# Performance work log

Measured on AMD Instinct MI355X. Metric: run time of the kernel, lower is better.

## Reference

```python
import jax, jax.numpy as jnp
import numpy as np

B, T, C, H = 2, 2048, 1024, 16
HD = C // H  # head_dim = 64


def setup_inputs() -> dict:
    key = jax.random.key(0)
    k1, k2, k3 = jax.random.split(key, 3)
    x = jax.random.normal(k1, (B, T, C), dtype=jnp.float32)
    w_attn = jax.random.normal(k2, (3 * C, C), dtype=jnp.float32) * 0.02
    w_proj = jax.random.normal(k3, (C, C), dtype=jnp.float32) * 0.02
    # RoPE frequencies: theta_i = 10000^(-2i/head_dim)
    inv_freq = 1.0 / (10000.0 ** (jnp.arange(0, HD, 2, dtype=jnp.float32) / HD))  # (HD//2,)
    angles = jnp.arange(T, dtype=jnp.float32)[:, None] * inv_freq[None, :]        # (T, HD//2)
    return {
        "x": x,
        "w_attn": w_attn,
        "w_proj": w_proj,
        "freqs_cos": jnp.cos(angles),
        "freqs_sin": jnp.sin(angles),
    }


def _rope(t, cos, sin):
    # t: (B, T, H, HD); cos/sin: (T, HD//2) broadcast to (1, T, 1, HD//2)
    te = t[..., 0::2]
    to = t[..., 1::2]
    c = cos[None, :, None, :]
    s = sin[None, :, None, :]
    re = te * c - to * s
    ro = te * s + to * c
    # interleave back: (..., HD//2, 2) -> (..., HD)
    return jnp.stack([re, ro], axis=-1).reshape(t.shape)


def reference(x, w_attn, w_proj, freqs_cos, freqs_sin):
    b, t, c = x.shape
    qkv = jnp.einsum('btc,fc->btf', x, w_attn)          # (B, T, 3C)
    q, k, v = jnp.split(qkv, 3, axis=2)
    q = q.reshape(b, t, H, HD)
    k = k.reshape(b, t, H, HD)
    v = v.reshape(b, t, H, HD)
    q = _rope(q, freqs_cos, freqs_sin)
    k = _rope(k, freqs_cos, freqs_sin)
    # causal SDPA
    scale = 1.0 / np.sqrt(HD).astype(np.float32)
    scores = jnp.einsum('bqhd,bkhd->bhqk', q, k) * scale  # (B, H, T, T)
    mask = jnp.tril(jnp.ones((t, t), dtype=bool))
    scores = jnp.where(mask[None, None, :, :], scores, jnp.finfo(scores.dtype).min)
    attn = jax.nn.softmax(scores, axis=-1)
    y = jnp.einsum('bhqk,bkhd->bqhd', attn, v).reshape(b, t, c)
    return jnp.einsum('btc,oc->bto', y, w_proj)
```

## Files before the change

kernel.cpp:

```cpp
#include <hip/hip_runtime.h>
#include <math.h>

#define B_  2
#define T_  2048
#define C_  1024
#define H_  16
#define HD_ 64
#define F3_ 3072

#define X4_   ((B_ * T_ * C_) / 4)
#define WA4_  ((F3_ * C_) / 4)
#define WP4_  ((C_ * C_) / 4)
#define TOT4_ (X4_ + WA4_ + WP4_)

typedef __attribute__((ext_vector_type(8))) __bf16 bf16x8;
typedef __attribute__((ext_vector_type(4))) float  f32x4;

__device__ __forceinline__ ushort f2bf(float f) {
  uint32_t u = __builtin_bit_cast(uint32_t, f);
  u += 0x7fff + ((u >> 16) & 1);
  return (ushort)(u >> 16);
}
__device__ __forceinline__ float bf2f(ushort u) {
  return __builtin_bit_cast(float, (uint32_t)u << 16);
}
__device__ __forceinline__ void gll16(void* lds, const void* g) {
  __builtin_amdgcn_global_load_lds(
      (const __attribute__((address_space(1))) void*)g,
      (__attribute__((address_space(3))) void*)lds, 16, 0, 0);
}

__global__ __launch_bounds__(256) void cvt_all(const float* __restrict__ x,
                                               const float* __restrict__ wa,
                                               const float* __restrict__ wp,
                                               ushort* __restrict__ out) {
  static_assert(X4_ == 1048576 && WA4_ == 786432 && WP4_ == 262144, "sizes");
  static_assert((X4_ % 256) == 0 && ((X4_ + WA4_) % 256) == 0, "block-uniform");
  int i = blockIdx.x * 256 + threadIdx.x;
  const float* src; int off;
  if (i < X4_)              { src = x;  off = i; }
  else if (i < X4_ + WA4_)  { src = wa; off = i - X4_; }
  else                      { src = wp; off = i - (X4_ + WA4_); }
  float4 v = ((const float4*)src)[off];
  ushort4 o;
  o.x = f2bf(v.x); o.y = f2bf(v.y); o.z = f2bf(v.z); o.w = f2bf(v.w);
  ((ushort4*)out)[i] = o;
}

template<int MODE>
__global__ __launch_bounds__(256) void gemm_mfma(
    const ushort* __restrict__ A, const ushort* __restrict__ Bm,
    void* __restrict__ Cout, ushort* __restrict__ vT,
    int M, int N, int K)
{
  __shared__ ushort As[128][64];
  __shared__ ushort Bs[128][64];
  const int tid  = threadIdx.x;
  const int lane = tid & 63, w = tid >> 6;
  const int wr = w >> 1, wc = w & 1;
  const int ll = lane & 15, lg = lane >> 4;
  const int r8 = lane >> 3;
  const int gc = ((lane & 7) ^ r8) << 3;
  const int m0 = blockIdx.x * 128, n0 = blockIdx.y * 128;

  f32x4 acc[4][4] = {};

  for (int k0 = 0; k0 < K; k0 += 64) {
    __syncthreads();
#pragma unroll
    for (int iss = 0; iss < 4; ++iss) {
      int rb = w * 32 + iss * 8;
      gll16(&As[rb][0], A  + (size_t)(m0 + rb + r8) * K + k0 + gc);
      gll16(&Bs[rb][0], Bm + (size_t)(n0 + rb + r8) * K + k0 + gc);
    }
    __syncthreads();
#pragma unroll
    for (int ks = 0; ks < 2; ++ks) {
      const int sw = ((ks * 4 + lg) ^ (ll & 7)) * 8;
      bf16x8 af[4], bfr[4];
#pragma unroll
      for (int mi = 0; mi < 4; ++mi)
        af[mi] = *(const bf16x8*)&As[wr * 64 + mi * 16 + ll][sw];
#pragma unroll
      for (int ni = 0; ni < 4; ++ni)
        bfr[ni] = *(const bf16x8*)&Bs[wc * 64 + ni * 16 + ll][sw];
      __builtin_amdgcn_s_setprio(1);
#pragma unroll
      for (int mi = 0; mi < 4; ++mi)
#pragma unroll
        for (int ni = 0; ni < 4; ++ni)
          acc[mi][ni] = __builtin_amdgcn_mfma_f32_16x16x32_bf16(
              af[mi], bfr[ni], acc[mi][ni], 0, 0, 0);
      __builtin_amdgcn_s_setprio(0);
    }
  }

  const int mrow = wr * 64 + lg * 4;
  const int ncol = wc * 64 + ll;
  if (MODE == 0) {
    float* C = (float*)Cout;
#pragma unroll
    for (int mi = 0; mi < 4; ++mi)
#pragma unroll
      for (int ni = 0; ni < 4; ++ni)
#pragma unroll
        for (int r = 0; r < 4; ++r)
          C[(size_t)(m0 + mrow + mi * 16 + r) * N + n0 + ncol + ni * 16] =
              acc[mi][ni][r];
  } else {
    if (n0 < 2 * C_) {
      ushort* q = (ushort*)Cout;
#pragma unroll
      for (int mi = 0; mi < 4; ++mi)
#pragma unroll
        for (int ni = 0; ni < 4; ++ni)
#pragma unroll
          for (int r = 0; r < 4; ++r)
            q[(size_t)(m0 + mrow + mi * 16 + r) * F3_ + n0 + ncol + ni * 16] =
                f2bf(acc[mi][ni][r]);
    } else {
      const int bb = m0 >> 11;
      const int tb = (m0 & 2047) + mrow;
#pragma unroll
      for (int mi = 0; mi < 4; ++mi)
#pragma unroll
        for (int ni = 0; ni < 4; ++ni) {
          int f  = n0 + ncol + ni * 16 - 2 * C_;
          int hh = f >> 6, d = f & 63;
          ushort4 o;
          o.x = f2bf(acc[mi][ni][0]); o.y = f2bf(acc[mi][ni][1]);
          o.z = f2bf(acc[mi][ni][2]); o.w = f2bf(acc[mi][ni][3]);
          *(ushort4*)&vT[(((size_t)(bb * H_ + hh) * HD_ + d) << 11) + tb + mi * 16] = o;
        }
    }
  }
}

#define QSC 0.18033688f
__global__ __launch_bounds__(256) void rope_bf(ushort* __restrict__ qkv,
                                               const float* __restrict__ fcos,
                                               const float* __restrict__ fsin) {
  int idx = blockIdx.x * 256 + threadIdx.x;
  int i2 = idx & 15;
  int h  = (idx >> 4) & 15;
  int t  = (idx >> 8) & 2047;
  int b  = idx >> 19;
  int fi = t * 32 + i2 * 2;
  float c0 = fcos[fi], s0 = fsin[fi], c1 = fcos[fi + 1], s1 = fsin[fi + 1];
  size_t base = (size_t)(b * T_ + t) * F3_ + h * HD_ + i2 * 4;
  ushort4 qv = *(ushort4*)&qkv[base];
  ushort4 qo;
  { float e = bf2f(qv.x), o = bf2f(qv.y);
    qo.x = f2bf((e * c0 - o * s0) * QSC);
    qo.y = f2bf((e * s0 + o * c0) * QSC); }
  { float e = bf2f(qv.z), o = bf2f(qv.w);
    qo.z = f2bf((e * c1 - o * s1) * QSC);
    qo.w = f2bf((e * s1 + o * c1) * QSC); }
  *(ushort4*)&qkv[base] = qo;
  ushort4 kv = *(ushort4*)&qkv[base + C_];
  ushort4 ko;
  { float e = bf2f(kv.x), o = bf2f(kv.y);
    ko.x = f2bf(e * c0 - o * s0);
    ko.y = f2bf(e * s0 + o * c0); }
  { float e = bf2f(kv.z), o = bf2f(kv.w);
    ko.z = f2bf(e * c1 - o * s1);
    ko.w = f2bf(e * s1 + o * c1); }
  *(ushort4*)&qkv[base + C_] = ko;
}

__global__ __launch_bounds__(256) void attn_mfma(
    const ushort* __restrict__ qkv, const ushort* __restrict__ vT,
    ushort* __restrict__ y)
{
  __shared__ __align__(16) ushort Qs[64][64];
  __shared__ __align__(16) ushort Ks[2][64][64], VTs[2][64][64];
  __shared__ __align__(16) ushort Ps[4][16][72];

  const int qt = 31 - blockIdx.y;
  const int bh = blockIdx.x;
  const int b = bh >> 4, h = bh & 15;
  const int q0 = qt * 64;
  const int tid = threadIdx.x, lane = tid & 63, w = tid >> 6;
  const int ll = lane & 15, lg = lane >> 4;
  const int r8 = lane >> 3;
  const int gc = ((lane & 7) ^ r8) << 3;
  const float NEG = -3.0e38f;

  const ushort* qb = qkv + (size_t)(b * T_) * F3_ + h * HD_;
  const ushort* kb = qb + C_;
  const ushort* vb = vT + ((size_t)(b * H_ + h) * HD_ << 11);

#pragma unroll
  for (int iss = 0; iss < 2; ++iss) {
    int rb = w * 16 + iss * 8;
    gll16(&Qs[rb][0], qb + (size_t)(q0 + rb + r8) * F3_ + gc);
    gll16(&Ks[0][rb][0],  kb + (size_t)(rb + r8) * F3_ + gc);
    gll16(&VTs[0][rb][0], vb + ((size_t)(rb + r8) << 11) + gc);
  }
  __syncthreads();

  bf16x8 qf[2];
#pragma unroll
  for (int ks = 0; ks < 2; ++ks)
    qf[ks] = *(const bf16x8*)&Qs[w * 16 + ll][((ks * 4 + lg) ^ (ll & 7)) * 8];

  f32x4 oacc[4] = {};
  float m_ = NEG, l_ = 0.f;
  int cur = 0;

  for (int kt = 0; kt <= qt; ++kt) {
    if (kt < qt) {
#pragma unroll
      for (int iss = 0; iss < 2; ++iss) {
        int rb = w * 16 + iss * 8;
        gll16(&Ks[cur ^ 1][rb][0],
              kb + (size_t)((kt + 1) * 64 + rb + r8) * F3_ + gc);
        gll16(&VTs[cur ^ 1][rb][0],
              vb + ((size_t)(rb + r8) << 11) + (kt + 1) * 64 + gc);
      }
    }

    f32x4 sacc[4] = {};
#pragma unroll
    for (int ks = 0; ks < 2; ++ks) {
      const int sw = ((ks * 4 + lg) ^ (ll & 7)) * 8;
      bf16x8 kf[4];
#pragma unroll
      for (int j = 0; j < 4; ++j)
        kf[j] = *(const bf16x8*)&Ks[cur][j * 16 + ll][sw];
      __builtin_amdgcn_s_setprio(1);
#pragma unroll
      for (int j = 0; j < 4; ++j)
        sacc[j] = __builtin_amdgcn_mfma_f32_16x16x32_bf16(kf[j], qf[ks], sacc[j], 0, 0, 0);
      __builtin_amdgcn_s_setprio(0);
    }

    if (kt == qt) {
#pragma unroll
      for (int j = 0; j < 4; ++j)
#pragma unroll
        for (int r = 0; r < 4; ++r)
          if (j * 16 + lg * 4 + r > w * 16 + ll) sacc[j][r] = NEG;
    }

    float tmax;
    {
      float t0 = fmaxf(fmaxf(sacc[0][0], sacc[0][1]), fmaxf(sacc[0][2], sacc[0][3]));
      float t1 = fmaxf(fmaxf(sacc[1][0], sacc[1][1]), fmaxf(sacc[1][2], sacc[1][3]));
      float t2 = fmaxf(fmaxf(sacc[2][0], sacc[2][1]), fmaxf(sacc[2][2], sacc[2][3]));
      float t3 = fmaxf(fmaxf(sacc[3][0], sacc[3][1]), fmaxf(sacc[3][2], sacc[3][3]));
      tmax = fmaxf(fmaxf(t0, t1), fmaxf(t2, t3));
      tmax = fmaxf(tmax, __shfl_xor(tmax, 16));
      tmax = fmaxf(tmax, __shfl_xor(tmax, 32));
    }
    if (!__all(tmax <= m_ + 11.5441f)) {
      float mnew = fmaxf(m_, tmax);
      float al = __builtin_amdgcn_exp2f(m_ - mnew);
      l_ *= al;
      m_ = mnew;
#pragma unroll
      for (int r = 0; r < 4; ++r) {
        float alr = __shfl(al, lg * 4 + r);
#pragma unroll
        for (int dj = 0; dj < 4; ++dj) oacc[dj][r] *= alr;
      }
    }
    float psum = 0.f;
#pragma unroll
    for (int j = 0; j < 4; ++j) {
      float p0 = __builtin_amdgcn_exp2f(sacc[j][0] - m_);
      float p1 = __builtin_amdgcn_exp2f(sacc[j][1] - m_);
      float p2 = __builtin_amdgcn_exp2f(sacc[j][2] - m_);
      float p3 = __builtin_amdgcn_exp2f(sacc[j][3] - m_);
      psum += (p0 + p1) + (p2 + p3);
      uint u0 = __builtin_bit_cast(uint32_t, p0) >> 16;
      uint u1 = __builtin_bit_cast(uint32_t, p1) & 0xffff0000u;
      uint u2 = __builtin_bit_cast(uint32_t, p2) >> 16;
      uint u3 = __builtin_bit_cast(uint32_t, p3) & 0xffff0000u;
      uint2 pk = make_uint2(u0 | u1, u2 | u3);
      *(uint2*)&Ps[w][ll][j * 16 + lg * 4] = pk;
    }
    psum += __shfl_xor(psum, 16);
    psum += __shfl_xor(psum, 32);
    l_ += psum;

#pragma unroll
    for (int ks = 0; ks < 2; ++ks) {
      bf16x8 pf = *(const bf16x8*)&Ps[w][ll][ks * 32 + lg * 8];
      const int sw = ((ks * 4 + lg) ^ (ll & 7)) * 8;
      bf16x8 vf[4];
#pragma unroll
      for (int dj = 0; dj < 4; ++dj)
        vf[dj] = *(const bf16x8*)&VTs[cur][dj * 16 + ll][sw];
      __builtin_amdgcn_s_setprio(1);
#pragma unroll
      for (int dj = 0; dj < 4; ++dj)
        oacc[dj] = __builtin_amdgcn_mfma_f32_16x16x32_bf16(pf, vf[dj], oacc[dj], 0, 0, 0);
      __builtin_amdgcn_s_setprio(0);
    }

    __syncthreads();
    cur ^= 1;
  }

#pragma unroll
  for (int r = 0; r < 4; ++r) {
    float lr = __shfl(l_, lg * 4 + r);
    float inv = 1.0f / lr;
    int row = q0 + w * 16 + lg * 4 + r;
#pragma unroll
    for (int dj = 0; dj < 4; ++dj)
      y[(size_t)(b * T_ + row) * C_ + h * HD_ + dj * 16 + ll] =
          f2bf(oacc[dj][r] * inv);
  }
}

extern "C" void kernel_launch(void* const* d_in, const int* in_sizes, int n_in,
                              void* d_out, int out_size, void* d_ws, size_t ws_size,
                              hipStream_t stream) {
  const float* x      = (const float*)d_in[0];
  const float* w_attn = (const float*)d_in[1];
  const float* w_proj = (const float*)d_in[2];
  const float* fcos   = (const float*)d_in[3];
  const float* fsin   = (const float*)d_in[4];
  float* out = (float*)d_out;

  ushort* xb   = (ushort*)d_ws;
  ushort* wab  = xb   + (size_t)4096 * 1024;
  ushort* wpb  = wab  + (size_t)3072 * 1024;
  ushort* qkvb = wpb  + (size_t)1024 * 1024;
  ushort* vt   = qkvb + (size_t)4096 * 3072;
  ushort* yb   = vt   + (size_t)32 * 64 * 2048;

  cvt_all<<<TOT4_ / 256, 256, 0, stream>>>(x, w_attn, w_proj, xb);

  { dim3 g(32, 24); gemm_mfma<1><<<g, 256, 0, stream>>>(xb, wab, qkvb, vt, 4096, F3_, C_); }
  rope_bf<<<4096, 256, 0, stream>>>(qkvb, fcos, fsin);
  { dim3 g(32, 32); attn_mfma<<<g, 256, 0, stream>>>(qkvb, vt, yb); }
  { dim3 g(32, 8);  gemm_mfma<0><<<g, 256, 0, stream>>>(yb, wpb, out, nullptr, 4096, C_, C_); }
}
```

Before: 109.9 us.

## Double-buffer GEMM LDS tiles with async global-to-LDS prefetch two tiles ahead

Converts the bf16 MFMA GEMM main loop from a single-buffered load/sync/compute pattern to a two-stage LDS ping-pong. The next tile's global-to-LDS loads are issued while MFMAs run on the current tile, with explicit vmcnt/lgkmcnt waits and barriers. The goal is to hide global memory latency behind compute. The cost is double the shared memory (64KB), which may lower occupancy, and a waitcnt schedule that is fragile to get right.

```diff
diff --git a/kernel.cpp b/kernel.cpp
--- a/kernel.cpp
+++ b/kernel.cpp
@@ -53,8 +53,8 @@
     void* __restrict__ Cout, ushort* __restrict__ vT,
     int M, int N, int K)
 {
-  __shared__ ushort As[128][64];
-  __shared__ ushort Bs[128][64];
+  __shared__ ushort As[2][128][64];
+  __shared__ ushort Bs[2][128][64];
   const int tid  = threadIdx.x;
   const int lane = tid & 63, w = tid >> 6;
   const int wr = w >> 1, wc = w & 1;
@@ -62,37 +62,66 @@
   const int r8 = lane >> 3;
   const int gc = ((lane & 7) ^ r8) << 3;
   const int m0 = blockIdx.x * 128, n0 = blockIdx.y * 128;
+  const int nt = K >> 6;
 
   f32x4 acc[4][4] = {};
 
-  for (int k0 = 0; k0 < K; k0 += 64) {
-    __syncthreads();
+#pragma unroll
+  for (int t = 0; t < 2; ++t)
 #pragma unroll
     for (int iss = 0; iss < 4; ++iss) {
       int rb = w * 32 + iss * 8;
-      gll16(&As[rb][0], A  + (size_t)(m0 + rb + r8) * K + k0 + gc);
-      gll16(&Bs[rb][0], Bm + (size_t)(n0 + rb + r8) * K + k0 + gc);
-    }
-    __syncthreads();
+      gll16(&As[t][rb][0], A  + (size_t)(m0 + rb + r8) * K + t * 64 + gc);
+      gll16(&Bs[t][rb][0], Bm + (size_t)(n0 + rb + r8) * K + t * 64 + gc);
+    }
+  asm volatile("s_waitcnt vmcnt(8)" ::: "memory");
+  __builtin_amdgcn_sched_barrier(0);
+  __builtin_amdgcn_s_barrier();
+
+  for (int kt = 0; kt < nt; ++kt) {
+    const int cur = kt & 1;
+    bf16x8 af[2][4], bfr[2][4];
 #pragma unroll
     for (int ks = 0; ks < 2; ++ks) {
       const int sw = ((ks * 4 + lg) ^ (ll & 7)) * 8;
-      bf16x8 af[4], bfr[4];
 #pragma unroll
       for (int mi = 0; mi < 4; ++mi)
-        af[mi] = *(const bf16x8*)&As[wr * 64 + mi * 16 + ll][sw];
+        af[ks][mi] = *(const bf16x8*)&As[cur][wr * 64 + mi * 16 + ll][sw];
 #pragma unroll
       for (int ni = 0; ni < 4; ++ni)
-        bfr[ni] = *(const bf16x8*)&Bs[wc * 64 + ni * 16 + ll][sw];
-      __builtin_amdgcn_s_setprio(1);
-#pragma unroll
-      for (int mi = 0; mi < 4; ++mi)
-#pragma unroll
-        for (int ni = 0; ni < 4; ++ni)
-          acc[mi][ni] = __builtin_amdgcn_mfma_f32_16x16x32_bf16(
-              af[mi], bfr[ni], acc[mi][ni], 0, 0, 0);
-      __builtin_amdgcn_s_setprio(0);
-    }
+        bfr[ks][ni] = *(const bf16x8*)&Bs[cur][wc * 64 + ni * 16 + ll][sw];
+    }
+    __builtin_amdgcn_s_setprio(1);
+#pragma unroll
+    for (int mi = 0; mi < 4; ++mi)
+#pragma unroll
+      for (int ni = 0; ni < 4; ++ni)
+        acc[mi][ni] = __builtin_amdgcn_mfma_f32_16x16x32_bf16(
+            af[0][mi], bfr[0][ni], acc[mi][ni], 0, 0, 0);
+    __builtin_amdgcn_s_setprio(0);
+    asm volatile("s_waitcnt lgkmcnt(0)" ::: "memory");
+    __builtin_amdgcn_sched_barrier(0);
+    __builtin_amdgcn_s_barrier();
+    if (kt + 2 < nt) {
+#pragma unroll
+      for (int iss = 0; iss < 4; ++iss) {
+        int rb = w * 32 + iss * 8;
+        gll16(&As[cur][rb][0], A  + (size_t)(m0 + rb + r8) * K + (kt + 2) * 64 + gc);
+        gll16(&Bs[cur][rb][0], Bm + (size_t)(n0 + rb + r8) * K + (kt + 2) * 64 + gc);
+      }
+    }
+    __builtin_amdgcn_s_setprio(1);
+#pragma unroll
+    for (int mi = 0; mi < 4; ++mi)
+#pragma unroll
+      for (int ni = 0; ni < 4; ++ni)
+        acc[mi][ni] = __builtin_amdgcn_mfma_f32_16x16x32_bf16(
+            af[1][mi], bfr[1][ni], acc[mi][ni], 0, 0, 0);
+    __builtin_amdgcn_s_setprio(0);
+    if (kt + 2 < nt) asm volatile("s_waitcnt vmcnt(8)" ::: "memory");
+    else             asm volatile("s_waitcnt vmcnt(0)" ::: "memory");
+    __builtin_amdgcn_sched_barrier(0);
+    __builtin_amdgcn_s_barrier();
   }
 
   const int mrow = wr * 64 + lg * 4;
```

Result: slower. 113.5 us (+3.3%).
